# Optimization experiments

Measured on AMD Instinct MI355X. Metric: run time of the kernel, lower is better.

The kernel has to match this reference:

```python
import jax, jax.numpy as jnp
import numpy as np

B, S, D, K = 4, 8192, 1024, 1024
TAU = 1.0  # gumbel-softmax temperature


def setup_inputs() -> dict:
    key = jax.random.key(0)
    k1, k2, k3 = jax.random.split(key, 3)
    embeddings = jax.random.normal(k1, (B, S, D), dtype=jnp.float32)
    codebook = jax.random.normal(k2, (K, D), dtype=jnp.float32) * 0.02
    # uniform noise in (0,1) for Gumbel sampling, same shape as logits [B,S,K]
    uniform_noise = jax.random.uniform(k3, (B, S, K), dtype=jnp.float32,
                                       minval=1e-6, maxval=1.0 - 1e-6)
    return {"embeddings": embeddings, "codebook": codebook,
            "uniform_noise": uniform_noise}


def reference(embeddings, codebook, uniform_noise):
    x2 = jnp.sum(embeddings * embeddings, axis=-1, keepdims=True)   # [B,S,1]
    c2 = jnp.sum(codebook * codebook, axis=-1)                      # [K]
    xc = jnp.einsum('bsd,kd->bsk', embeddings, codebook)            # [B,S,K]
    d2 = jnp.maximum(x2 + c2 - 2.0 * xc, 0.0)
    logits = -jnp.sqrt(d2)                                          # [B,S,K]
    # Gumbel-softmax (training path, hard=False)
    gumbel = -jnp.log(-jnp.log(uniform_noise))
    weights = jax.nn.softmax((logits + gumbel) / TAU, axis=-1)      # [B,S,K]
    quantized = jnp.einsum('bsk,kd->bsd', weights, codebook)        # [B,S,D]
    return quantized, logits
```

## Files before the change

kernel.cpp:

```cpp
#include <hip/hip_runtime.h>
#include <hip/hip_bf16.h>

constexpr int MM   = 32768;
constexpr int NN   = 1024;
constexpr int KRED = 1024;
constexpr int LDAB = KRED * 2;

using s16x8 = __attribute__((ext_vector_type(8))) short;
using f32x4 = __attribute__((ext_vector_type(4))) float;

__device__ __forceinline__ unsigned short f2bf(float f) {
  unsigned u = __float_as_uint(f);
  return (unsigned short)((u + 0x7fffu + ((u >> 16) & 1u)) >> 16);
}

__device__ __forceinline__ void gload_lds16(const void* g, void* l) {
  __builtin_amdgcn_global_load_lds(
      (const __attribute__((address_space(1))) void*)g,
      (__attribute__((address_space(3))) void*)l, 16, 0, 0);
}

__device__ __forceinline__ float wave_sum(float v) {
#pragma unroll
  for (int o = 32; o > 0; o >>= 1) v += __shfl_xor(v, o);
  return v;
}
__device__ __forceinline__ float wave_max(float v) {
#pragma unroll
  for (int o = 32; o > 0; o >>= 1) v = fmaxf(v, __shfl_xor(v, o));
  return v;
}

__global__ __launch_bounds__(256) void prep_cb(const float* __restrict__ C,
                                               unsigned short* __restrict__ CB,
                                               unsigned short* __restrict__ CT,
                                               float* __restrict__ c2) {
  int k = blockIdx.x;
  int t = threadIdx.x;
  const float4 v = *(const float4*)(C + (size_t)k * 1024 + t * 4);
  ushort4 b = make_ushort4(f2bf(v.x), f2bf(v.y), f2bf(v.z), f2bf(v.w));
  *(ushort4*)(CB + (size_t)k * 1024 + t * 4) = b;
  CT[(size_t)(t * 4 + 0) * 1024 + k] = b.x;
  CT[(size_t)(t * 4 + 1) * 1024 + k] = b.y;
  CT[(size_t)(t * 4 + 2) * 1024 + k] = b.z;
  CT[(size_t)(t * 4 + 3) * 1024 + k] = b.w;
  float p = v.x * v.x + v.y * v.y + v.z * v.z + v.w * v.w;
  p = wave_sum(p);
  __shared__ float red[4];
  if ((t & 63) == 0) red[t >> 6] = p;
  __syncthreads();
  if (t == 0) c2[k] = red[0] + red[1] + red[2] + red[3];
}

__global__ __launch_bounds__(512) void prep_x(const float* __restrict__ X,
                                              unsigned short* __restrict__ Xb,
                                              float* __restrict__ x2) {
  int tid = threadIdx.x;
  int l = tid & 63, w = tid >> 6;
  int m = blockIdx.x * 8 + w;
  size_t base = (size_t)m * 1024 + l * 4;
  float p = 0.0f;
#pragma unroll
  for (int j = 0; j < 4; ++j) {
    const float4 v = *(const float4*)(X + base + j * 256);
    *(ushort4*)(Xb + base + j * 256) =
        make_ushort4(f2bf(v.x), f2bf(v.y), f2bf(v.z), f2bf(v.w));
    p += v.x * v.x + v.y * v.y + v.z * v.z + v.w * v.w;
  }
  p = wave_sum(p);
  if (l == 0) x2[m] = p;
}

__global__ __launch_bounds__(512) void softmax_k(const float* __restrict__ logits,
                                                 const float* __restrict__ noise,
                                                 unsigned short* __restrict__ W) {
  int tid = threadIdx.x;
  int l = tid & 63, w = tid >> 6;
  int m = blockIdx.x * 8 + w;
  size_t base = (size_t)m * 1024 + l * 4;

  float s[16];
  float mx = -3.0e38f;
#pragma unroll
  for (int j = 0; j < 4; ++j) {
    const float4 lv = *(const float4*)(logits + base + j * 256);
    const float4 nv = *(const float4*)(noise + base + j * 256);
    s[j * 4 + 0] = lv.x - __logf(-logf(nv.x));
    s[j * 4 + 1] = lv.y - __logf(-logf(nv.y));
    s[j * 4 + 2] = lv.z - __logf(-logf(nv.z));
    s[j * 4 + 3] = lv.w - __logf(-logf(nv.w));
    mx = fmaxf(mx, fmaxf(fmaxf(s[j * 4], s[j * 4 + 1]),
                         fmaxf(s[j * 4 + 2], s[j * 4 + 3])));
  }
  mx = wave_max(mx);

  float ps = 0.0f;
#pragma unroll
  for (int i = 0; i < 16; ++i) {
    s[i] = __expf(s[i] - mx);
    ps += s[i];
  }
  ps = wave_sum(ps);
  float inv = 1.0f / ps;

#pragma unroll
  for (int j = 0; j < 4; ++j) {
    *(ushort4*)(W + base + j * 256) =
        make_ushort4(f2bf(s[j * 4 + 0] * inv), f2bf(s[j * 4 + 1] * inv),
                     f2bf(s[j * 4 + 2] * inv), f2bf(s[j * 4 + 3] * inv));
  }
}

template <int MODE>
__global__ __launch_bounds__(512, 2) void gemm256(const unsigned short* __restrict__ A,
                                                  const unsigned short* __restrict__ Bt,
                                                  float* __restrict__ out,
                                                  const float* __restrict__ x2,
                                                  const float* __restrict__ c2) {
  extern __shared__ char smem[];

  int bid = blockIdx.x;
  int swz = (bid & 7) * 64 + (bid >> 3);
  int bm = swz >> 2, bn = swz & 3;
  int brow0 = bm * 256, bcol0 = bn * 256;

  int tid = threadIdx.x;
  int l = tid & 63, w = tid >> 6;
  int wm = w >> 2, wn = w & 3;
  int lr = l & 15, lh = l >> 4;
  const int xsw = (lr & 7) << 4;

  const char* AbH[2] = { (const char*)A + (size_t)brow0 * LDAB,
                         (const char*)A + (size_t)(brow0 + 128) * LDAB };
  const char* BbH[2] = { (const char*)Bt + (size_t)bcol0 * LDAB,
                         (const char*)Bt + (size_t)(bcol0 + 128) * LDAB };

  const int sr0 = tid >> 3;
  const int sc  = (tid & 7) * 16;
  const int scx0 = sc ^ ((sr0 & 7) << 4);

#define STAGE(gbase, kbyte, ldsreg)                                            \
  do {                                                                         \
    gload_lds16((gbase) + (size_t)sr0 * LDAB + (kbyte) + scx0,                 \
                (ldsreg) + tid * 16);                                          \
    gload_lds16((gbase) + (size_t)(sr0 + 64) * LDAB + (kbyte) + scx0,          \
                (ldsreg) + 8192 + tid * 16);                                   \
  } while (0)

  STAGE(AbH[0], 0, smem + 0);
  STAGE(AbH[1], 0, smem + 16384);
  STAGE(BbH[0], 0, smem + 32768);
  STAGE(BbH[1], 0, smem + 49152);
  STAGE(BbH[0], 128, smem + 65536 + 32768);
  STAGE(BbH[1], 128, smem + 65536 + 49152);
  asm volatile("s_waitcnt vmcnt(4)" ::: "memory");
  __builtin_amdgcn_s_barrier();

  const int aoff0 = wm * 16384 + lr * 128;
  const int boff0 = (wn >> 1) * 16384 + (wn & 1) * 8192 + lr * 128;

  f32x4 acc[8][4] = {};
  s16x8 af[4][2], bf[4][2];

#pragma unroll 2
  for (int t = 0; t < 16; ++t) {
    int p = t & 1;
    char* As  = smem + p * 65536;
    char* Bs  = smem + p * 65536 + 32768;
    char* Asn = smem + (1 - p) * 65536;

#pragma unroll
    for (int mi = 0; mi < 4; ++mi)
#pragma unroll
      for (int ks = 0; ks < 2; ++ks)
        af[mi][ks] = *(const s16x8*)(As + aoff0 + mi * 2048 + ((ks * 64 + lh * 16) ^ xsw));
#pragma unroll
    for (int ni = 0; ni < 2; ++ni)
#pragma unroll
      for (int ks = 0; ks < 2; ++ks)
        bf[ni][ks] = *(const s16x8*)(Bs + boff0 + ni * 2048 + ((ks * 64 + lh * 16) ^ xsw));
    if (t + 1 < 16) STAGE(AbH[0], (t + 1) * 128, Asn + 0);
    __builtin_amdgcn_s_barrier();
    asm volatile("s_waitcnt lgkmcnt(0)" ::: "memory");
    __builtin_amdgcn_sched_barrier(0);
    __builtin_amdgcn_s_setprio(1);
#pragma unroll
    for (int mi = 0; mi < 4; ++mi)
#pragma unroll
      for (int ni = 0; ni < 2; ++ni)
#pragma unroll
        for (int ks = 0; ks < 2; ++ks)
          acc[mi][ni] = __builtin_amdgcn_mfma_f32_16x16x32_bf16(af[mi][ks], bf[ni][ks], acc[mi][ni], 0, 0, 0);
    __builtin_amdgcn_s_setprio(0);
    __builtin_amdgcn_s_barrier();

#pragma unroll
    for (int ni = 0; ni < 2; ++ni)
#pragma unroll
      for (int ks = 0; ks < 2; ++ks)
        bf[2 + ni][ks] = *(const s16x8*)(Bs + boff0 + (2 + ni) * 2048 + ((ks * 64 + lh * 16) ^ xsw));
    if (t + 1 < 16) STAGE(AbH[1], (t + 1) * 128, Asn + 16384);
    __builtin_amdgcn_s_barrier();
    asm volatile("s_waitcnt lgkmcnt(0)" ::: "memory");
    __builtin_amdgcn_sched_barrier(0);
    __builtin_amdgcn_s_setprio(1);
#pragma unroll
    for (int mi = 0; mi < 4; ++mi)
#pragma unroll
      for (int ni = 0; ni < 2; ++ni)
#pragma unroll
        for (int ks = 0; ks < 2; ++ks)
          acc[mi][2 + ni] = __builtin_amdgcn_mfma_f32_16x16x32_bf16(af[mi][ks], bf[2 + ni][ks], acc[mi][2 + ni], 0, 0, 0);
    __builtin_amdgcn_s_setprio(0);
    __builtin_amdgcn_s_barrier();

#pragma unroll
    for (int mi = 0; mi < 4; ++mi)
#pragma unroll
      for (int ks = 0; ks < 2; ++ks)
        af[mi][ks] = *(const s16x8*)(As + aoff0 + (4 + mi) * 2048 + ((ks * 64 + lh * 16) ^ xsw));
    if (t + 2 < 16) STAGE(BbH[0], (t + 2) * 128, Bs + 0);
    __builtin_amdgcn_s_barrier();
    asm volatile("s_waitcnt lgkmcnt(0)" ::: "memory");
    __builtin_amdgcn_sched_barrier(0);
    __builtin_amdgcn_s_setprio(1);
#pragma unroll
    for (int mi = 0; mi < 4; ++mi)
#pragma unroll
      for (int ni = 0; ni < 2; ++ni)
#pragma unroll
        for (int ks = 0; ks < 2; ++ks)
          acc[4 + mi][ni] = __builtin_amdgcn_mfma_f32_16x16x32_bf16(af[mi][ks], bf[ni][ks], acc[4 + mi][ni], 0, 0, 0);
    __builtin_amdgcn_s_setprio(0);
    __builtin_amdgcn_s_barrier();

    if (t + 2 < 16) STAGE(BbH[1], (t + 2) * 128, Bs + 16384);
    __builtin_amdgcn_s_setprio(1);
#pragma unroll
    for (int mi = 0; mi < 4; ++mi)
#pragma unroll
      for (int ni = 0; ni < 2; ++ni)
#pragma unroll
        for (int ks = 0; ks < 2; ++ks)
          acc[4 + mi][2 + ni] = __builtin_amdgcn_mfma_f32_16x16x32_bf16(af[mi][ks], bf[2 + ni][ks], acc[4 + mi][2 + ni], 0, 0, 0);
    __builtin_amdgcn_s_setprio(0);
    __builtin_amdgcn_sched_barrier(0);
    if (t < 14) { asm volatile("s_waitcnt vmcnt(4)" ::: "memory"); }
    else        { asm volatile("s_waitcnt vmcnt(0)" ::: "memory"); }
    __builtin_amdgcn_s_barrier();
  }
#undef STAGE

#pragma unroll
  for (int mi = 0; mi < 8; ++mi) {
    int row0 = brow0 + wm * 128 + mi * 16 + lh * 4;
#pragma unroll
    for (int r = 0; r < 4; ++r) {
      int row = row0 + r;
      float xv = (MODE == 1) ? x2[row] : 0.0f;
#pragma unroll
      for (int ni = 0; ni < 4; ++ni) {
        int col = bcol0 + wn * 64 + ni * 16 + lr;
        float v = acc[mi][ni][r];
        if (MODE == 1) {
          float d2 = xv + c2[col] - 2.0f * v;
          v = -sqrtf(fmaxf(d2, 0.0f));
        }
        out[(size_t)row * NN + col] = v;
      }
    }
  }
}

extern "C" void kernel_launch(void* const* d_in, const int* in_sizes, int n_in,
                              void* d_out, int out_size, void* d_ws, size_t ws_size,
                              hipStream_t stream) {
  const float* emb   = (const float*)d_in[0];
  const float* cb    = (const float*)d_in[1];
  const float* noise = (const float*)d_in[2];

  float* quant  = (float*)d_out;
  float* logits = (float*)d_out + (size_t)MM * NN;

  char* ws = (char*)d_ws;
  unsigned short* XW = (unsigned short*)ws;
  unsigned short* CB = (unsigned short*)(ws + 67108864);
  unsigned short* CT = (unsigned short*)(ws + 69206016);
  float* x2 = (float*)(ws + 71303168);
  float* c2 = (float*)(ws + 71434240);

  static bool attr_done = false;
  if (!attr_done) {
    hipFuncSetAttribute((const void*)gemm256<1>,
                        hipFuncAttributeMaxDynamicSharedMemorySize, 131072);
    hipFuncSetAttribute((const void*)gemm256<0>,
                        hipFuncAttributeMaxDynamicSharedMemorySize, 131072);
    attr_done = true;
  }

  prep_cb<<<dim3(1024), dim3(256), 0, stream>>>(cb, CB, CT, c2);
  prep_x<<<dim3(MM / 8), dim3(512), 0, stream>>>(emb, XW, x2);
  gemm256<1><<<dim3(512), dim3(512), 131072, stream>>>(XW, CB, logits, x2, c2);
  softmax_k<<<dim3(MM / 8), dim3(512), 0, stream>>>(logits, noise, XW);
  gemm256<0><<<dim3(512), dim3(512), 131072, stream>>>(XW, CT, quant, nullptr, nullptr);
}
```

Baseline: 257.5 us.

## Fuse Gumbel-softmax into second GEMM's A-tile staging with analytic max bound

Removes the standalone softmax kernel and computes the unnormalized Gumbel-softmax weights inside the second GEMM while staging A tiles. Logits and noise are loaded from global memory, turned into bf16 exp values written to LDS, and row sums are accumulated so the output is divided by the sum in the epilogue. The row max is replaced by a fixed bound (8 - sqrt(x2)), which avoids a separate max pass but risks overflow or underflow if the Gumbel noise or distances exceed that bound. Each of the four column blocks recomputes the log/exp for the same rows, so transcendental work is duplicated fourfold. In exchange, the bf16 weight matrix no longer has to be written to and read back from global memory.

```diff
diff --git a/kernel.cpp b/kernel.cpp
--- a/kernel.cpp
+++ b/kernel.cpp
@@ -23,11 +23,6 @@
 __device__ __forceinline__ float wave_sum(float v) {
 #pragma unroll
   for (int o = 32; o > 0; o >>= 1) v += __shfl_xor(v, o);
-  return v;
-}
-__device__ __forceinline__ float wave_max(float v) {
-#pragma unroll
-  for (int o = 32; o > 0; o >>= 1) v = fmaxf(v, __shfl_xor(v, o));
   return v;
 }
 
@@ -71,46 +66,6 @@
   if (l == 0) x2[m] = p;
 }
 
-__global__ __launch_bounds__(512) void softmax_k(const float* __restrict__ logits,
-                                                 const float* __restrict__ noise,
-                                                 unsigned short* __restrict__ W) {
-  int tid = threadIdx.x;
-  int l = tid & 63, w = tid >> 6;
-  int m = blockIdx.x * 8 + w;
-  size_t base = (size_t)m * 1024 + l * 4;
-
-  float s[16];
-  float mx = -3.0e38f;
-#pragma unroll
-  for (int j = 0; j < 4; ++j) {
-    const float4 lv = *(const float4*)(logits + base + j * 256);
-    const float4 nv = *(const float4*)(noise + base + j * 256);
-    s[j * 4 + 0] = lv.x - __logf(-logf(nv.x));
-    s[j * 4 + 1] = lv.y - __logf(-logf(nv.y));
-    s[j * 4 + 2] = lv.z - __logf(-logf(nv.z));
-    s[j * 4 + 3] = lv.w - __logf(-logf(nv.w));
-    mx = fmaxf(mx, fmaxf(fmaxf(s[j * 4], s[j * 4 + 1]),
-                         fmaxf(s[j * 4 + 2], s[j * 4 + 3])));
-  }
-  mx = wave_max(mx);
-
-  float ps = 0.0f;
-#pragma unroll
-  for (int i = 0; i < 16; ++i) {
-    s[i] = __expf(s[i] - mx);
-    ps += s[i];
-  }
-  ps = wave_sum(ps);
-  float inv = 1.0f / ps;
-
-#pragma unroll
-  for (int j = 0; j < 4; ++j) {
-    *(ushort4*)(W + base + j * 256) =
-        make_ushort4(f2bf(s[j * 4 + 0] * inv), f2bf(s[j * 4 + 1] * inv),
-                     f2bf(s[j * 4 + 2] * inv), f2bf(s[j * 4 + 3] * inv));
-  }
-}
-
 template <int MODE>
 __global__ __launch_bounds__(512, 2) void gemm256(const unsigned short* __restrict__ A,
                                                   const unsigned short* __restrict__ Bt,
@@ -272,6 +227,241 @@
   }
 }
 
+__global__ __launch_bounds__(512, 2) void gemm2f(const float* __restrict__ logits,
+                                                 const float* __restrict__ noise,
+                                                 const unsigned short* __restrict__ Bt,
+                                                 const float* __restrict__ x2,
+                                                 float* __restrict__ out) {
+  extern __shared__ char smem[];
+
+  int bid = blockIdx.x;
+  int swz = (bid & 7) * 64 + (bid >> 3);
+  int bm = swz >> 2, bn = swz & 3;
+  int brow0 = bm * 256, bcol0 = bn * 256;
+
+  int tid = threadIdx.x;
+  int l = tid & 63, w = tid >> 6;
+  int wm = w >> 2, wn = w & 3;
+  int lr = l & 15, lh = l >> 4;
+  const int xsw = (lr & 7) << 4;
+
+  const char* BbH[2] = { (const char*)Bt + (size_t)bcol0 * LDAB,
+                         (const char*)Bt + (size_t)(bcol0 + 128) * LDAB };
+
+  const int sr0 = tid >> 3;
+  const int sc  = (tid & 7) * 16;
+  const int scx0 = sc ^ ((sr0 & 7) << 4);
+
+  const float C00 = 8.0f - sqrtf(x2[brow0 + sr0]);
+  const float C01 = 8.0f - sqrtf(x2[brow0 + 64 + sr0]);
+  const float C10 = 8.0f - sqrtf(x2[brow0 + 128 + sr0]);
+  const float C11 = 8.0f - sqrtf(x2[brow0 + 192 + sr0]);
+  float ls00 = 0.0f, ls01 = 0.0f, ls10 = 0.0f, ls11 = 0.0f;
+
+  const char* Lp = (const char*)logits;
+  const char* Np = (const char*)noise;
+  const size_t ro = ((size_t)(brow0 + sr0) << 12) + (size_t)((tid & 7) << 5);
+  const int wbase = sr0 * 128 + scx0;
+
+  float4 vL0a, vL0b, vL1a, vL1b, vN0a, vN0b, vN1a, vN1b;
+
+#define AISSUE(h, t1)                                                          \
+  do {                                                                         \
+    size_t o = ro + (size_t)(h) * 524288 + (size_t)(t1) * 256;                 \
+    vL0a = *(const float4*)(Lp + o);                                           \
+    vL0b = *(const float4*)(Lp + o + 16);                                      \
+    vL1a = *(const float4*)(Lp + o + 262144);                                  \
+    vL1b = *(const float4*)(Lp + o + 262144 + 16);                             \
+    vN0a = *(const float4*)(Np + o);                                           \
+    vN0b = *(const float4*)(Np + o + 16);                                      \
+    vN1a = *(const float4*)(Np + o + 262144);                                  \
+    vN1b = *(const float4*)(Np + o + 262144 + 16);                             \
+  } while (0)
+
+#define CVT8(LA, LB, NA, NB, Cc, LS, DST)                                      \
+  do {                                                                         \
+    float p0 = __expf((LA.x - logf(-logf(NA.x))) - (Cc));                      \
+    float p1 = __expf((LA.y - logf(-logf(NA.y))) - (Cc));                      \
+    float p2 = __expf((LA.z - logf(-logf(NA.z))) - (Cc));                      \
+    float p3 = __expf((LA.w - logf(-logf(NA.w))) - (Cc));                      \
+    float p4 = __expf((LB.x - logf(-logf(NB.x))) - (Cc));                      \
+    float p5 = __expf((LB.y - logf(-logf(NB.y))) - (Cc));                      \
+    float p6 = __expf((LB.z - logf(-logf(NB.z))) - (Cc));                      \
+    float p7 = __expf((LB.w - logf(-logf(NB.w))) - (Cc));                      \
+    (LS) += p0 + p1 + p2 + p3 + p4 + p5 + p6 + p7;                             \
+    int4 dw;                                                                   \
+    dw.x = (int)f2bf(p0) | ((int)f2bf(p1) << 16);                              \
+    dw.y = (int)f2bf(p2) | ((int)f2bf(p3) << 16);                              \
+    dw.z = (int)f2bf(p4) | ((int)f2bf(p5) << 16);                              \
+    dw.w = (int)f2bf(p6) | ((int)f2bf(p7) << 16);                              \
+    *(int4*)(DST) = dw;                                                        \
+  } while (0)
+
+#define STAGEB(gbase, kbyte, ldsreg)                                           \
+  do {                                                                         \
+    gload_lds16((gbase) + (size_t)sr0 * LDAB + (kbyte) + scx0,                 \
+                (ldsreg) + tid * 16);                                          \
+    gload_lds16((gbase) + (size_t)(sr0 + 64) * LDAB + (kbyte) + scx0,          \
+                (ldsreg) + 8192 + tid * 16);                                   \
+  } while (0)
+
+  AISSUE(0, 0);
+  STAGEB(BbH[0], 0, smem + 32768);
+  STAGEB(BbH[1], 0, smem + 49152);
+  asm volatile("s_waitcnt vmcnt(4)" ::: "memory");
+  CVT8(vL0a, vL0b, vN0a, vN0b, C00, ls00, smem + wbase);
+  CVT8(vL1a, vL1b, vN1a, vN1b, C01, ls01, smem + 8192 + wbase);
+  AISSUE(1, 0);
+  STAGEB(BbH[0], 128, smem + 65536 + 32768);
+  STAGEB(BbH[1], 128, smem + 65536 + 49152);
+  asm volatile("s_waitcnt vmcnt(4)" ::: "memory");
+  CVT8(vL0a, vL0b, vN0a, vN0b, C10, ls10, smem + 16384 + wbase);
+  CVT8(vL1a, vL1b, vN1a, vN1b, C11, ls11, smem + 16384 + 8192 + wbase);
+  asm volatile("s_waitcnt lgkmcnt(0)" ::: "memory");
+  __builtin_amdgcn_s_barrier();
+
+  const int aoff0 = wm * 16384 + lr * 128;
+  const int boff0 = (wn >> 1) * 16384 + (wn & 1) * 8192 + lr * 128;
+
+  f32x4 acc[8][4] = {};
+  s16x8 af[4][2], bf[4][2];
+
+#pragma unroll 2
+  for (int t = 0; t < 16; ++t) {
+    int p = t & 1;
+    char* As  = smem + p * 65536;
+    char* Bs  = smem + p * 65536 + 32768;
+    char* Asn = smem + (1 - p) * 65536;
+
+#pragma unroll
+    for (int mi = 0; mi < 4; ++mi)
+#pragma unroll
+      for (int ks = 0; ks < 2; ++ks)
+        af[mi][ks] = *(const s16x8*)(As + aoff0 + mi * 2048 + ((ks * 64 + lh * 16) ^ xsw));
+#pragma unroll
+    for (int ni = 0; ni < 2; ++ni)
+#pragma unroll
+      for (int ks = 0; ks < 2; ++ks)
+        bf[ni][ks] = *(const s16x8*)(Bs + boff0 + ni * 2048 + ((ks * 64 + lh * 16) ^ xsw));
+    if (t + 1 < 16) AISSUE(0, t + 1);
+    __builtin_amdgcn_s_barrier();
+    asm volatile("s_waitcnt lgkmcnt(0)" ::: "memory");
+    __builtin_amdgcn_sched_barrier(0);
+    __builtin_amdgcn_s_setprio(1);
+#pragma unroll
+    for (int mi = 0; mi < 4; ++mi)
+#pragma unroll
+      for (int ni = 0; ni < 2; ++ni)
+#pragma unroll
+        for (int ks = 0; ks < 2; ++ks)
+          acc[mi][ni] = __builtin_amdgcn_mfma_f32_16x16x32_bf16(af[mi][ks], bf[ni][ks], acc[mi][ni], 0, 0, 0);
+    __builtin_amdgcn_s_setprio(0);
+    __builtin_amdgcn_s_barrier();
+
+#pragma unroll
+    for (int ni = 0; ni < 2; ++ni)
+#pragma unroll
+      for (int ks = 0; ks < 2; ++ks)
+        bf[2 + ni][ks] = *(const s16x8*)(Bs + boff0 + (2 + ni) * 2048 + ((ks * 64 + lh * 16) ^ xsw));
+    if (t + 1 < 16) {
+      asm volatile("s_waitcnt vmcnt(0)" ::: "memory");
+      CVT8(vL0a, vL0b, vN0a, vN0b, C00, ls00, Asn + wbase);
+      CVT8(vL1a, vL1b, vN1a, vN1b, C01, ls01, Asn + 8192 + wbase);
+      AISSUE(1, t + 1);
+    }
+    __builtin_amdgcn_s_barrier();
+    asm volatile("s_waitcnt lgkmcnt(0)" ::: "memory");
+    __builtin_amdgcn_sched_barrier(0);
+    __builtin_amdgcn_s_setprio(1);
+#pragma unroll
+    for (int mi = 0; mi < 4; ++mi)
+#pragma unroll
+      for (int ni = 0; ni < 2; ++ni)
+#pragma unroll
+        for (int ks = 0; ks < 2; ++ks)
+          acc[mi][2 + ni] = __builtin_amdgcn_mfma_f32_16x16x32_bf16(af[mi][ks], bf[2 + ni][ks], acc[mi][2 + ni], 0, 0, 0);
+    __builtin_amdgcn_s_setprio(0);
+    __builtin_amdgcn_s_barrier();
+
+#pragma unroll
+    for (int mi = 0; mi < 4; ++mi)
+#pragma unroll
+      for (int ks = 0; ks < 2; ++ks)
+        af[mi][ks] = *(const s16x8*)(As + aoff0 + (4 + mi) * 2048 + ((ks * 64 + lh * 16) ^ xsw));
+    if (t + 2 < 16) STAGEB(BbH[0], (t + 2) * 128, Bs + 0);
+    __builtin_amdgcn_s_barrier();
+    asm volatile("s_waitcnt lgkmcnt(0)" ::: "memory");
+    __builtin_amdgcn_sched_barrier(0);
+    __builtin_amdgcn_s_setprio(1);
+#pragma unroll
+    for (int mi = 0; mi < 4; ++mi)
+#pragma unroll
+      for (int ni = 0; ni < 2; ++ni)
+#pragma unroll
+        for (int ks = 0; ks < 2; ++ks)
+          acc[4 + mi][ni] = __builtin_amdgcn_mfma_f32_16x16x32_bf16(af[mi][ks], bf[ni][ks], acc[4 + mi][ni], 0, 0, 0);
+    __builtin_amdgcn_s_setprio(0);
+    __builtin_amdgcn_s_barrier();
+
+    if (t + 2 < 16) STAGEB(BbH[1], (t + 2) * 128, Bs + 16384);
+    if (t + 1 < 16) {
+      if (t < 14) { asm volatile("s_waitcnt vmcnt(4)" ::: "memory"); }
+      else        { asm volatile("s_waitcnt vmcnt(0)" ::: "memory"); }
+      CVT8(vL0a, vL0b, vN0a, vN0b, C10, ls10, Asn + 16384 + wbase);
+      CVT8(vL1a, vL1b, vN1a, vN1b, C11, ls11, Asn + 16384 + 8192 + wbase);
+    }
+    __builtin_amdgcn_s_setprio(1);
+#pragma unroll
+    for (int mi = 0; mi < 4; ++mi)
+#pragma unroll
+      for (int ni = 0; ni < 2; ++ni)
+#pragma unroll
+        for (int ks = 0; ks < 2; ++ks)
+          acc[4 + mi][2 + ni] = __builtin_amdgcn_mfma_f32_16x16x32_bf16(af[mi][ks], bf[2 + ni][ks], acc[4 + mi][2 + ni], 0, 0, 0);
+    __builtin_amdgcn_s_setprio(0);
+    __builtin_amdgcn_sched_barrier(0);
+    asm volatile("s_waitcnt lgkmcnt(0)" ::: "memory");
+    if (t < 14) { asm volatile("s_waitcnt vmcnt(4)" ::: "memory"); }
+    else        { asm volatile("s_waitcnt vmcnt(0)" ::: "memory"); }
+    __builtin_amdgcn_s_barrier();
+  }
+#undef STAGEB
+#undef AISSUE
+#undef CVT8
+
+  float v00 = ls00, v01 = ls01, v10 = ls10, v11 = ls11;
+#pragma unroll
+  for (int o = 1; o <= 4; o <<= 1) {
+    v00 += __shfl_xor(v00, o);
+    v01 += __shfl_xor(v01, o);
+    v10 += __shfl_xor(v10, o);
+    v11 += __shfl_xor(v11, o);
+  }
+  float* l_lds = (float*)smem;
+  if ((tid & 7) == 0) {
+    l_lds[sr0]       = v00;
+    l_lds[64 + sr0]  = v01;
+    l_lds[128 + sr0] = v10;
+    l_lds[192 + sr0] = v11;
+  }
+  __syncthreads();
+
+#pragma unroll
+  for (int mi = 0; mi < 8; ++mi) {
+    int rl0 = wm * 128 + mi * 16 + lh * 4;
+#pragma unroll
+    for (int r = 0; r < 4; ++r) {
+      int rl = rl0 + r;
+      float inv = 1.0f / l_lds[rl];
+#pragma unroll
+      for (int ni = 0; ni < 4; ++ni) {
+        int col = bcol0 + wn * 64 + ni * 16 + lr;
+        out[(size_t)(brow0 + rl) * NN + col] = acc[mi][ni][r] * inv;
+      }
+    }
+  }
+}
+
 extern "C" void kernel_launch(void* const* d_in, const int* in_sizes, int n_in,
                               void* d_out, int out_size, void* d_ws, size_t ws_size,
                               hipStream_t stream) {
@@ -293,7 +483,7 @@
   if (!attr_done) {
     hipFuncSetAttribute((const void*)gemm256<1>,
                         hipFuncAttributeMaxDynamicSharedMemorySize, 131072);
-    hipFuncSetAttribute((const void*)gemm256<0>,
+    hipFuncSetAttribute((const void*)gemm2f,
                         hipFuncAttributeMaxDynamicSharedMemorySize, 131072);
     attr_done = true;
   }
@@ -301,6 +491,5 @@
   prep_cb<<<dim3(1024), dim3(256), 0, stream>>>(cb, CB, CT, c2);
   prep_x<<<dim3(MM / 8), dim3(512), 0, stream>>>(emb, XW, x2);
   gemm256<1><<<dim3(512), dim3(512), 131072, stream>>>(XW, CB, logits, x2, c2);
-  softmax_k<<<dim3(MM / 8), dim3(512), 0, stream>>>(logits, noise, XW);
-  gemm256<0><<<dim3(512), dim3(512), 131072, stream>>>(XW, CT, quant, nullptr, nullptr);
-}
+  gemm2f<<<dim3(512), dim3(512), 131072, stream>>>(logits, noise, CT, x2, quant);
+}
```

Result: slower. 569.7 us (+121.2%).

## Fuse Gumbel-softmax into distance GEMM epilogue with deferred row normalisation

Applied to the files above, without the earlier changes.

Removes the standalone softmax kernel. The first GEMM's epilogue now reads the noise, computes unnormalised exp weights against a fixed per-row bound (8 - sqrt(|x|^2)) instead of the true row max, and writes them as bf16. It also writes per-column-block partial row sums, and the second GEMM scales its output by the inverse of the summed partials. This saves a full re-read of the logits and one launch, at the cost of uncoalesced epilogue noise loads and 2-byte stores, plus reliance on the bound keeping exp in range.

```diff
diff --git a/kernel.cpp b/kernel.cpp
--- a/kernel.cpp
+++ b/kernel.cpp
@@ -23,11 +23,6 @@
 __device__ __forceinline__ float wave_sum(float v) {
 #pragma unroll
   for (int o = 32; o > 0; o >>= 1) v += __shfl_xor(v, o);
-  return v;
-}
-__device__ __forceinline__ float wave_max(float v) {
-#pragma unroll
-  for (int o = 32; o > 0; o >>= 1) v = fmaxf(v, __shfl_xor(v, o));
   return v;
 }
 
@@ -71,52 +66,15 @@
   if (l == 0) x2[m] = p;
 }
 
-__global__ __launch_bounds__(512) void softmax_k(const float* __restrict__ logits,
-                                                 const float* __restrict__ noise,
-                                                 unsigned short* __restrict__ W) {
-  int tid = threadIdx.x;
-  int l = tid & 63, w = tid >> 6;
-  int m = blockIdx.x * 8 + w;
-  size_t base = (size_t)m * 1024 + l * 4;
-
-  float s[16];
-  float mx = -3.0e38f;
-#pragma unroll
-  for (int j = 0; j < 4; ++j) {
-    const float4 lv = *(const float4*)(logits + base + j * 256);
-    const float4 nv = *(const float4*)(noise + base + j * 256);
-    s[j * 4 + 0] = lv.x - __logf(-logf(nv.x));
-    s[j * 4 + 1] = lv.y - __logf(-logf(nv.y));
-    s[j * 4 + 2] = lv.z - __logf(-logf(nv.z));
-    s[j * 4 + 3] = lv.w - __logf(-logf(nv.w));
-    mx = fmaxf(mx, fmaxf(fmaxf(s[j * 4], s[j * 4 + 1]),
-                         fmaxf(s[j * 4 + 2], s[j * 4 + 3])));
-  }
-  mx = wave_max(mx);
-
-  float ps = 0.0f;
-#pragma unroll
-  for (int i = 0; i < 16; ++i) {
-    s[i] = __expf(s[i] - mx);
-    ps += s[i];
-  }
-  ps = wave_sum(ps);
-  float inv = 1.0f / ps;
-
-#pragma unroll
-  for (int j = 0; j < 4; ++j) {
-    *(ushort4*)(W + base + j * 256) =
-        make_ushort4(f2bf(s[j * 4 + 0] * inv), f2bf(s[j * 4 + 1] * inv),
-                     f2bf(s[j * 4 + 2] * inv), f2bf(s[j * 4 + 3] * inv));
-  }
-}
-
 template <int MODE>
 __global__ __launch_bounds__(512, 2) void gemm256(const unsigned short* __restrict__ A,
                                                   const unsigned short* __restrict__ Bt,
                                                   float* __restrict__ out,
                                                   const float* __restrict__ x2,
-                                                  const float* __restrict__ c2) {
+                                                  const float* __restrict__ c2,
+                                                  const float* __restrict__ noise,
+                                                  unsigned short* __restrict__ W,
+                                                  float* __restrict__ lpart) {
   extern __shared__ char smem[];
 
   int bid = blockIdx.x;
@@ -251,22 +209,62 @@
   }
 #undef STAGE
 
-#pragma unroll
-  for (int mi = 0; mi < 8; ++mi) {
-    int row0 = brow0 + wm * 128 + mi * 16 + lh * 4;
-#pragma unroll
-    for (int r = 0; r < 4; ++r) {
-      int row = row0 + r;
-      float xv = (MODE == 1) ? x2[row] : 0.0f;
-#pragma unroll
-      for (int ni = 0; ni < 4; ++ni) {
-        int col = bcol0 + wn * 64 + ni * 16 + lr;
-        float v = acc[mi][ni][r];
-        if (MODE == 1) {
+  if (MODE == 1) {
+    float* rs = (float*)smem;
+#pragma unroll
+    for (int mi = 0; mi < 8; ++mi) {
+      int rl0 = wm * 128 + mi * 16 + lh * 4;
+#pragma unroll
+      for (int r = 0; r < 4; ++r) {
+        int rl = rl0 + r;
+        int row = brow0 + rl;
+        float xv = x2[row];
+        float Crow = 8.0f - sqrtf(xv);
+        float rowp = 0.0f;
+#pragma unroll
+        for (int ni = 0; ni < 4; ++ni) {
+          int col = bcol0 + wn * 64 + ni * 16 + lr;
+          float v = acc[mi][ni][r];
           float d2 = xv + c2[col] - 2.0f * v;
-          v = -sqrtf(fmaxf(d2, 0.0f));
+          float lg = -sqrtf(fmaxf(d2, 0.0f));
+          out[(size_t)row * NN + col] = lg;
+          float u = noise[(size_t)row * NN + col];
+          float pp = __expf(lg - __logf(-__logf(u)) - Crow);
+          W[(size_t)row * NN + col] = f2bf(pp);
+          rowp += pp;
         }
-        out[(size_t)row * NN + col] = v;
+#pragma unroll
+        for (int o = 1; o <= 8; o <<= 1) rowp += __shfl_xor(rowp, o);
+        if (lr == 0) rs[wn * 256 + rl] = rowp;
+      }
+    }
+    __syncthreads();
+    if (tid < 256) {
+      float ls = rs[tid] + rs[256 + tid] + rs[512 + tid] + rs[768 + tid];
+      lpart[(size_t)bn * MM + brow0 + tid] = ls;
+    }
+  } else {
+    __syncthreads();
+    float* invl = (float*)smem;
+    if (tid < 256) {
+      int row = brow0 + tid;
+      float ls = lpart[row] + lpart[MM + row] + lpart[2 * MM + row] +
+                 lpart[3 * MM + row];
+      invl[tid] = 1.0f / ls;
+    }
+    __syncthreads();
+#pragma unroll
+    for (int mi = 0; mi < 8; ++mi) {
+      int rl0 = wm * 128 + mi * 16 + lh * 4;
+#pragma unroll
+      for (int r = 0; r < 4; ++r) {
+        int rl = rl0 + r;
+        float inv = invl[rl];
+#pragma unroll
+        for (int ni = 0; ni < 4; ++ni) {
+          int col = bcol0 + wn * 64 + ni * 16 + lr;
+          out[(size_t)(brow0 + rl) * NN + col] = acc[mi][ni][r] * inv;
+        }
       }
     }
   }
@@ -283,11 +281,13 @@
   float* logits = (float*)d_out + (size_t)MM * NN;
 
   char* ws = (char*)d_ws;
-  unsigned short* XW = (unsigned short*)ws;
-  unsigned short* CB = (unsigned short*)(ws + 67108864);
-  unsigned short* CT = (unsigned short*)(ws + 69206016);
-  float* x2 = (float*)(ws + 71303168);
-  float* c2 = (float*)(ws + 71434240);
+  unsigned short* Xb = (unsigned short*)ws;
+  unsigned short* W  = (unsigned short*)(ws + 67108864);
+  unsigned short* CB = (unsigned short*)(ws + 134217728);
+  unsigned short* CT = (unsigned short*)(ws + 136314880);
+  float* x2    = (float*)(ws + 138412032);
+  float* c2    = (float*)(ws + 138543104);
+  float* lpart = (float*)(ws + 138547200);
 
   static bool attr_done = false;
   if (!attr_done) {
@@ -299,8 +299,10 @@
   }
 
   prep_cb<<<dim3(1024), dim3(256), 0, stream>>>(cb, CB, CT, c2);
-  prep_x<<<dim3(MM / 8), dim3(512), 0, stream>>>(emb, XW, x2);
-  gemm256<1><<<dim3(512), dim3(512), 131072, stream>>>(XW, CB, logits, x2, c2);
-  softmax_k<<<dim3(MM / 8), dim3(512), 0, stream>>>(logits, noise, XW);
-  gemm256<0><<<dim3(512), dim3(512), 131072, stream>>>(XW, CT, quant, nullptr, nullptr);
-}
+  prep_x<<<dim3(MM / 8), dim3(512), 0, stream>>>(emb, Xb, x2);
+  gemm256<1><<<dim3(512), dim3(512), 131072, stream>>>(Xb, CB, logits, x2, c2,
+                                                       noise, W, lpart);
+  gemm256<0><<<dim3(512), dim3(512), 131072, stream>>>(W, CT, quant, nullptr,
+                                                       nullptr, nullptr, nullptr,
+                                                       lpart);
+}
```

Result: slower. 279.1 us (+8.4%).
